# Kernel optimization log

Hardware: AMD Instinct MI355X
Metric: run time of the kernel (lower is better)

Reference implementation:

```python
import jax, jax.numpy as jnp
import numpy as np
from jax import lax

B, S, C = 32, 512, 32          # batch, seq_len (words), char_len
V, E = 101, 64                 # char vocab (printable + pad), emb size
F, K = 128, 3                  # n_filters, kernel_size


def setup_inputs() -> dict:
    key = jax.random.key(0)
    k0, k1, k2, k3 = jax.random.split(key, 4)
    char_ids = jax.random.randint(k0, (B, S, C), 0, V, dtype=jnp.int32)
    emb_table = jax.random.normal(k1, (V, E), dtype=jnp.float32)
    emb_table = emb_table.at[0].set(0.0)  # padding_idx=0
    fan_in = E * K
    conv_w = jax.random.normal(k2, (F, E, K), dtype=jnp.float32) / np.sqrt(fan_in)
    conv_b = jax.random.normal(k3, (F,), dtype=jnp.float32) * 0.01
    return {"char_ids": char_ids, "emb_table": emb_table,
            "conv_w": conv_w, "conv_b": conv_b}


def reference(char_ids, emb_table, conv_w, conv_b):
    b, s, c = char_ids.shape
    e = emb_table.shape[1]
    # embedding lookup: [B, S, C, E]; dropout p=0.0 (eval) -> identity
    char_embs = emb_table[char_ids]
    # FAITHFUL to torch source: .view(-1, E, C) is a raw row-major
    # reinterpretation of the contiguous [B*S, C, E] buffer (not a permute).
    x = char_embs.reshape(b * s, e, c)  # [B*S, E, C] by memory layout
    # Conv1d over the last axis, valid padding
    y = lax.conv_general_dilated(
        x, conv_w, window_strides=(1,), padding="VALID",
        dimension_numbers=("NCH", "OIH", "NCH"))  # [B*S, F, C-K+1]
    y = y + conv_b[None, :, None]
    # max-pool over time, then back to [B, S, F]
    return y.max(axis=2).reshape(b, s, -1)
```

## Files before the change

### kernel.cpp

```cpp
#include <hip/hip_runtime.h>
#include <cstdint>


typedef __bf16 bf16x8 __attribute__((ext_vector_type(8)));
typedef float  f32x16 __attribute__((ext_vector_type(16)));

#define NW   16
#define WPW  8
#define ROWS 34
#define RST  72

__global__ __launch_bounds__(256)
void prep_pack(const float* __restrict__ w, const float* __restrict__ emb,
               __bf16* __restrict__ pw, uint32_t* __restrict__ Dt) {
  int i = blockIdx.x * 256 + threadIdx.x;
  if (i < 24576) {
    int j    = i & 7;
    int lane = (i >> 3) & 63;
    int ks   = (i >> 9) & 3;
    int t    = i >> 11;
    int kk   = t % 3;
    int nt   = t / 3;
    int f = nt * 32 + (lane & 31);
    int e = ks * 16 + (lane >> 5) * 8 + j;
    pw[i] = (__bf16)w[f * 192 + e * 3 + kk];
  } else if (i < 24576 + 3232) {
    int i2 = i - 24576;
    int c = i2 >> 5, r = i2 & 31;
    uint32_t lo = (uint32_t)__builtin_bit_cast(uint16_t, (__bf16)emb[c * 64 + r]);
    uint32_t hi = (uint32_t)__builtin_bit_cast(uint16_t, (__bf16)emb[c * 64 + 32 + r]);
    Dt[i2] = (hi << 16) | lo;
  }
}

__global__ __launch_bounds__(256, 2)
void charcnn_mfma(const int* __restrict__ cid, const uint32_t* __restrict__ Dt,
                  const float* __restrict__ bias, const __bf16* __restrict__ pw,
                  float* __restrict__ out) {
  __shared__ __align__(16) __bf16 xT[4][2][ROWS * RST];

  const int tid  = threadIdx.x;
  const int lane = tid & 63;
  const int wv   = tid >> 6;
  const int np   = wv & 1;
  const int ws   = wv >> 1;

  bf16x8 bfrag[2][12];
  const bf16x8* pwv = (const bf16x8*)pw;
#pragma unroll
  for (int nt = 0; nt < 2; ++nt)
#pragma unroll
    for (int q = 0; q < 12; ++q)
      bfrag[nt][q] = pwv[((np * 2 + nt) * 12 + q) * 64 + lane];

  const float vb0 = bias[(np * 2 + 0) * 32 + (lane & 31)];
  const float vb1 = bias[(np * 2 + 1) * 32 + (lane & 31)];

  const int bw = blockIdx.x * NW;

  int c0[WPW];
#pragma unroll
  for (int j = 0; j < WPW; ++j)
    c0[j] = cid[(bw + ws + 2 * j) * 32 + (lane & 31)];

  const int sa = lane >> 1;
  const int ss = lane & 1;

  uint4 sd[4];

  auto stage_load = [&](int j) {
    int ch = __shfl(c0[j], lane >> 1);
    const uint4* row = (const uint4*)(Dt + ch * 32) + ss * 4;
#pragma unroll
    for (int q = 0; q < 4; ++q) sd[q] = row[q];
  };

  auto stage_write = [&](__bf16* buf) {
    uint32_t* d = (uint32_t*)buf + sa;
#pragma unroll
    for (int q = 0; q < 4; ++q) {
      d[(16 * ss + q * 4 + 0) * 36] = sd[q].x;
      d[(16 * ss + q * 4 + 1) * 36] = sd[q].y;
      d[(16 * ss + q * 4 + 2) * 36] = sd[q].z;
      d[(16 * ss + q * 4 + 3) * 36] = sd[q].w;
    }
  };

  auto finish = [&](const f32x16& acc, float vbv, int fcol, int w) {
    float m01 = fmaxf(acc[0],  acc[1]);
    float m23 = fmaxf(acc[2],  acc[3]);
    float m45 = fmaxf(acc[4],  acc[5]);
    float m67 = fmaxf(acc[6],  acc[7]);
    float m89 = fmaxf(acc[8],  acc[9]);
    float mab = fmaxf(acc[10], acc[11]);
    float mcd = fmaxf(acc[12], acc[13]);
    float q0 = fmaxf(m01, m23);
    float q1 = fmaxf(m45, m67);
    float q2 = fmaxf(m89, mab);
    float m0 = fmaxf(fmaxf(q0, q1), fmaxf(q2, mcd));
    float m1 = fmaxf(acc[14], acc[15]);
    float mm = (lane < 32) ? fmaxf(m0, m1) : m0;
    float other = __shfl_xor(mm, 32, 64);
    float fullmax = fmaxf(mm, other) + vbv;
    if (lane < 32) out[(bw + w) * 128 + fcol + lane] = fullmax;
  };

  auto compute_word = [&](int w, const __bf16* buf) {
    const __bf16* xb = buf + (lane & 31) * RST + (lane >> 5) * 8;
    f32x16 acc0, acc1;
#pragma unroll
    for (int r = 0; r < 16; ++r) { acc0[r] = 0.0f; acc1[r] = 0.0f; }

#pragma unroll
    for (int kk = 0; kk < 3; ++kk) {
#pragma unroll
      for (int ks = 0; ks < 4; ++ks) {
        bf16x8 av = *(const bf16x8*)(xb + kk * RST + ks * 16);
        acc0 = __builtin_amdgcn_mfma_f32_32x32x16_bf16(av, bfrag[0][kk * 4 + ks],
                                                       acc0, 0, 0, 0);
        acc1 = __builtin_amdgcn_mfma_f32_32x32x16_bf16(av, bfrag[1][kk * 4 + ks],
                                                       acc1, 0, 0, 0);
      }
    }
    finish(acc0, vb0, np * 64,      w);
    finish(acc1, vb1, np * 64 + 32, w);
  };

  stage_load(0);
  stage_write(&xT[wv][0][0]);

#pragma unroll
  for (int j = 0; j < WPW; ++j) {
    if (j + 1 < WPW) stage_load(j + 1);
    compute_word(ws + 2 * j, &xT[wv][j & 1][0]);
    if (j + 1 < WPW) stage_write(&xT[wv][(j + 1) & 1][0]);
  }
}

extern "C" void kernel_launch(void* const* d_in, const int* in_sizes, int n_in,
                              void* d_out, int out_size, void* d_ws, size_t ws_size,
                              hipStream_t stream) {
  const int*   cid = (const int*)d_in[0];
  const float* emb = (const float*)d_in[1];
  const float* cw  = (const float*)d_in[2];
  const float* cb  = (const float*)d_in[3];
  float* outp = (float*)d_out;
  __bf16*   pw = (__bf16*)d_ws;
  uint32_t* Dt = (uint32_t*)((char*)d_ws + 49152);

  hipLaunchKernelGGL(prep_pack, dim3(109), dim3(256), 0, stream, cw, emb, pw, Dt);
  hipLaunchKernelGGL(charcnn_mfma, dim3(1024), dim3(256), 0, stream,
                     cid, Dt, cb, pw, outp);
}
```

Before: 34.96 us.

## Fuse weight and embedding packing into main kernel using shared-memory tables

Removes the separate prep_pack launch. Each block now converts the conv weights to bf16 MFMA fragment order and builds the bf16 embedding table in shared memory. The per-word embedding gather reads from an XOR-swizzled shared table instead of global memory. This saves one kernel launch and the global round trip for the gather, but every one of the 1024 blocks repeats about 24K weight conversions with strided global reads before any compute starts.

```diff
diff --git a/kernel.cpp b/kernel.cpp
--- a/kernel.cpp
+++ b/kernel.cpp
@@ -4,64 +4,74 @@
 
 typedef __bf16 bf16x8 __attribute__((ext_vector_type(8)));
 typedef float  f32x16 __attribute__((ext_vector_type(16)));
+typedef uint32_t u32;
 
 #define NW   16
 #define WPW  8
 #define ROWS 34
 #define RST  72
-
-__global__ __launch_bounds__(256)
-void prep_pack(const float* __restrict__ w, const float* __restrict__ emb,
-               __bf16* __restrict__ pw, uint32_t* __restrict__ Dt) {
-  int i = blockIdx.x * 256 + threadIdx.x;
-  if (i < 24576) {
-    int j    = i & 7;
-    int lane = (i >> 3) & 63;
-    int ks   = (i >> 9) & 3;
-    int t    = i >> 11;
-    int kk   = t % 3;
-    int nt   = t / 3;
-    int f = nt * 32 + (lane & 31);
-    int e = ks * 16 + (lane >> 5) * 8 + j;
-    pw[i] = (__bf16)w[f * 192 + e * 3 + kk];
-  } else if (i < 24576 + 3232) {
-    int i2 = i - 24576;
-    int c = i2 >> 5, r = i2 & 31;
-    uint32_t lo = (uint32_t)__builtin_bit_cast(uint16_t, (__bf16)emb[c * 64 + r]);
-    uint32_t hi = (uint32_t)__builtin_bit_cast(uint16_t, (__bf16)emb[c * 64 + 32 + r]);
-    Dt[i2] = (hi << 16) | lo;
-  }
-}
+#define XT_BYTES 39168
+#define SMEM_BYTES 52096
 
 __global__ __launch_bounds__(256, 2)
-void charcnn_mfma(const int* __restrict__ cid, const uint32_t* __restrict__ Dt,
-                  const float* __restrict__ bias, const __bf16* __restrict__ pw,
+void charcnn_mfma(const int* __restrict__ cid, const float* __restrict__ emb,
+                  const float* __restrict__ bias, const float* __restrict__ wraw,
                   float* __restrict__ out) {
-  __shared__ __align__(16) __bf16 xT[4][2][ROWS * RST];
+  __shared__ __align__(16) char smem[SMEM_BYTES];
+  __bf16* pwL = (__bf16*)smem;
+  u32*    DtL = (u32*)(smem + XT_BYTES);
 
   const int tid  = threadIdx.x;
   const int lane = tid & 63;
   const int wv   = tid >> 6;
   const int np   = wv & 1;
   const int ws   = wv >> 1;
-
-  bf16x8 bfrag[2][12];
-  const bf16x8* pwv = (const bf16x8*)pw;
-#pragma unroll
-  for (int nt = 0; nt < 2; ++nt)
-#pragma unroll
-    for (int q = 0; q < 12; ++q)
-      bfrag[nt][q] = pwv[((np * 2 + nt) * 12 + q) * 64 + lane];
-
-  const float vb0 = bias[(np * 2 + 0) * 32 + (lane & 31)];
-  const float vb1 = bias[(np * 2 + 1) * 32 + (lane & 31)];
-
-  const int bw = blockIdx.x * NW;
+  const int bw   = blockIdx.x * NW;
 
   int c0[WPW];
 #pragma unroll
   for (int j = 0; j < WPW; ++j)
     c0[j] = cid[(bw + ws + 2 * j) * 32 + (lane & 31)];
+
+  {
+    u32* pw32 = (u32*)pwL;
+    for (int h = tid; h < 12288; h += 256) {
+      int I    = h << 1;
+      int j    = I & 7;
+      int l    = (I >> 3) & 63;
+      int ks   = (I >> 9) & 3;
+      int t    = I >> 11;
+      int kk   = t % 3;
+      int nt   = t / 3;
+      int f = nt * 32 + (l & 31);
+      int e = ks * 16 + (l >> 5) * 8 + j;
+      float w0 = wraw[f * 192 + e * 3 + kk];
+      float w1 = wraw[f * 192 + (e + 1) * 3 + kk];
+      u32 u = ((u32)__builtin_bit_cast(uint16_t, (__bf16)w1) << 16)
+            |  (u32)__builtin_bit_cast(uint16_t, (__bf16)w0);
+      pw32[h] = u;
+    }
+  }
+  __syncthreads();
+
+  bf16x8 bfrag[2][12];
+#pragma unroll
+  for (int nt = 0; nt < 2; ++nt)
+#pragma unroll
+    for (int q = 0; q < 12; ++q)
+      bfrag[nt][q] = *(const bf16x8*)(pwL + ((((np * 2 + nt) * 12 + q) * 64 + lane) << 3));
+  __syncthreads();
+
+  for (int h = tid; h < 3232; h += 256) {
+    int c = h >> 5, r = h & 31;
+    u32 lo = (u32)__builtin_bit_cast(uint16_t, (__bf16)emb[c * 64 + r]);
+    u32 hi = (u32)__builtin_bit_cast(uint16_t, (__bf16)emb[c * 64 + 32 + r]);
+    DtL[(c << 5) | (r ^ ((c & 7) << 2))] = (hi << 16) | lo;
+  }
+
+  const float vb0 = bias[(np * 2 + 0) * 32 + (lane & 31)];
+  const float vb1 = bias[(np * 2 + 1) * 32 + (lane & 31)];
+  __syncthreads();
 
   const int sa = lane >> 1;
   const int ss = lane & 1;
@@ -69,14 +79,16 @@
   uint4 sd[4];
 
   auto stage_load = [&](int j) {
-    int ch = __shfl(c0[j], lane >> 1);
-    const uint4* row = (const uint4*)(Dt + ch * 32) + ss * 4;
+    int ch = __shfl(c0[j], sa);
+    const u32* base = DtL + (ch << 5);
+    const int  sw   = (ch & 7) << 2;
 #pragma unroll
-    for (int q = 0; q < 4; ++q) sd[q] = row[q];
+    for (int q = 0; q < 4; ++q)
+      sd[q] = *(const uint4*)(base + ((ss * 16 + q * 4) ^ sw));
   };
 
   auto stage_write = [&](__bf16* buf) {
-    uint32_t* d = (uint32_t*)buf + sa;
+    u32* d = (u32*)buf + sa;
 #pragma unroll
     for (int q = 0; q < 4; ++q) {
       d[(16 * ss + q * 4 + 0) * 36] = sd[q].x;
@@ -126,14 +138,17 @@
     finish(acc1, vb1, np * 64 + 32, w);
   };
 
+  __bf16* xb0 = (__bf16*)(smem + wv * 2 * 4896);
+  __bf16* xb1 = (__bf16*)(smem + (wv * 2 + 1) * 4896);
+
   stage_load(0);
-  stage_write(&xT[wv][0][0]);
+  stage_write(xb0);
 
 #pragma unroll
   for (int j = 0; j < WPW; ++j) {
     if (j + 1 < WPW) stage_load(j + 1);
-    compute_word(ws + 2 * j, &xT[wv][j & 1][0]);
-    if (j + 1 < WPW) stage_write(&xT[wv][(j + 1) & 1][0]);
+    compute_word(ws + 2 * j, (j & 1) ? xb1 : xb0);
+    if (j + 1 < WPW) stage_write((j & 1) ? xb0 : xb1);
   }
 }
 
@@ -145,10 +160,8 @@
   const float* cw  = (const float*)d_in[2];
   const float* cb  = (const float*)d_in[3];
   float* outp = (float*)d_out;
-  __bf16*   pw = (__bf16*)d_ws;
-  uint32_t* Dt = (uint32_t*)((char*)d_ws + 49152);
+  (void)d_ws; (void)ws_size;
 
-  hipLaunchKernelGGL(prep_pack, dim3(109), dim3(256), 0, stream, cw, emb, pw, Dt);
   hipLaunchKernelGGL(charcnn_mfma, dim3(1024), dim3(256), 0, stream,
-                     cid, Dt, cb, pw, outp);
+                     cid, emb, cb, cw, outp);
 }
```

Result: slower. 67.63 us (+93.4%).
